# Kernel tuning notes

Measured on AMD Instinct MI355X. Metric: run time of the kernel, lower is better.

Reference implementation:

```python
import jax, jax.numpy as jnp
import numpy as np

N = 64
L = 4096
STEP = 0.001


def _make_dplr_hippo(n):
    # Standard S4 DPLR HiPPO-LegS construction (numpy, done once at setup).
    q = np.arange(n, dtype=np.float64)
    col = np.sqrt(1.0 + 2.0 * q)
    A = -(np.tril(col[:, None] * col[None, :]) - np.diag(q))
    P = np.sqrt(q + 0.5)
    B = np.sqrt(2.0 * q + 1.0)
    S = A + P[:, None] * P[None, :]
    lam_re = np.mean(np.diag(S)) * np.ones(n)
    lam_im, V = np.linalg.eigh(S * -1j)
    Pc = V.conj().T @ P
    Bc = V.conj().T @ B
    return lam_re, lam_im, Pc, Bc


def setup_inputs() -> dict:
    key = jax.random.key(0)
    k1, k2 = jax.random.split(key)
    x = jax.random.normal(k1, (16, 256, L), dtype=jnp.float32)
    lam_re, lam_im, Pc, Bc = _make_dplr_hippo(N)
    Cp = np.asarray(jax.random.normal(k2, (N, 2), dtype=jnp.float32)) * 0.5 ** 0.5
    return {
        "x": x,
        "Lambda_re": jnp.asarray(lam_re, dtype=jnp.float32),
        "Lambda_im": jnp.asarray(lam_im, dtype=jnp.float32),
        "P_re": jnp.asarray(Pc.real, dtype=jnp.float32),
        "P_im": jnp.asarray(Pc.imag, dtype=jnp.float32),
        "B_re": jnp.asarray(Bc.real, dtype=jnp.float32),
        "B_im": jnp.asarray(Bc.imag, dtype=jnp.float32),
        "C_re": jnp.asarray(Cp[:, 0], dtype=jnp.float32),
        "C_im": jnp.asarray(Cp[:, 1], dtype=jnp.float32),
    }


def _fourier_kernel(Lambda, P, B, C, step, length):
    # Frequency-domain DPLR SSM kernel (Annotated-S4 kernel_DPLR, at the roots of unity).
    Omega = jnp.exp(-2j * jnp.pi * jnp.arange(length) / length).astype(jnp.complex64)  # [L]
    g = (2.0 / step) * ((1.0 - Omega) / (1.0 + Omega))  # bilinear-transform frequencies [L]
    c = 2.0 / (1.0 + Omega)
    denom = 1.0 / (g[:, None] - Lambda[None, :])  # Cauchy matrix [L, N]
    k00 = denom @ (jnp.conj(C) * B)
    k01 = denom @ (jnp.conj(C) * P)
    k10 = denom @ (jnp.conj(P) * B)  # Q = P in this module
    k11 = denom @ (jnp.conj(P) * P)
    return c * (k00 - k01 * (1.0 / (1.0 + k11)) * k10)  # [L] complex64


def reference(x, Lambda_re, Lambda_im, P_re, P_im, B_re, B_im, C_re, C_im):
    Lambda = (Lambda_re + 1j * Lambda_im).astype(jnp.complex64)
    P = (P_re + 1j * P_im).astype(jnp.complex64)
    B = (B_re + 1j * B_im).astype(jnp.complex64)
    C = (C_re + 1j * C_im).astype(jnp.complex64)
    K = _fourier_kernel(Lambda, P, B, C, STEP, L)  # [L]
    fft_u = jnp.fft.fft(x, n=L)                    # [batch, ch, L] complex64
    y = jnp.fft.ifft(K * fft_u, n=L)
    return y.real.astype(x.dtype)
```

## Files before the change

### kernel.cpp

```cpp
#include <hip/hip_runtime.h>
#include <math.h>

#define LEN 4096
#define NSTATE 64

__device__ inline float2 cmulf(float2 a, float2 b){
  return make_float2(a.x*b.x - a.y*b.y, a.x*b.y + a.y*b.x);
}

__global__ __launch_bounds__(64)
void s4_kernelA1(const float* __restrict__ Lre, const float* __restrict__ Lim,
                 const float* __restrict__ Pre, const float* __restrict__ Pim,
                 const float* __restrict__ Bre, const float* __restrict__ Bim,
                 const float* __restrict__ Cre, const float* __restrict__ Cim,
                 float2* __restrict__ Kout) {
  const int k = blockIdx.x;
  const int n = threadIdx.x;

  double ang = -2.0 * M_PI * (double)k / (double)LEN;
  double orr = cos(ang), oi = sin(ang);
  double dr = 1.0 + orr, di = oi;
  double d2 = dr*dr + di*di;
  double nr = 1.0 - orr, ni = -oi;
  double inv_d2 = 1.0 / d2;
  double gr = 2000.0 * (nr*dr + ni*di) * inv_d2;
  double gi = 2000.0 * (ni*dr - nr*di) * inv_d2;
  double cr = 2.0 * dr * inv_d2, ci = -2.0 * di * inv_d2;

  double lr = Lre[n], li = Lim[n];
  double pr = Pre[n], pi = Pim[n];
  double br = Bre[n], bi = Bim[n];
  double qr = Cre[n], qi = Cim[n];
  double er = gr - lr, ei = gi - li;
  double inv_e2 = 1.0 / (er*er + ei*ei);
  double den_r = er * inv_e2, den_i = -ei * inv_e2;
  double cbr = qr*br + qi*bi, cbi = qr*bi - qi*br;
  double cpr = qr*pr + qi*pi, cpi = qr*pi - qi*pr;
  double pbr = pr*br + pi*bi, pbi = pr*bi - pi*br;
  double ppr = pr*pr + pi*pi;

  double k00r = den_r*cbr - den_i*cbi, k00i = den_r*cbi + den_i*cbr;
  double k01r = den_r*cpr - den_i*cpi, k01i = den_r*cpi + den_i*cpr;
  double k10r = den_r*pbr - den_i*pbi, k10i = den_r*pbi + den_i*pbr;
  double k11r = den_r*ppr,             k11i = den_i*ppr;

  #pragma unroll
  for (int off = 32; off >= 1; off >>= 1) {
    k00r += __shfl_xor(k00r, off); k00i += __shfl_xor(k00i, off);
    k01r += __shfl_xor(k01r, off); k01i += __shfl_xor(k01i, off);
    k10r += __shfl_xor(k10r, off); k10i += __shfl_xor(k10i, off);
    k11r += __shfl_xor(k11r, off); k11i += __shfl_xor(k11i, off);
  }

  if (n == 0) {
    double ar = 1.0 + k11r, ai = k11i;
    double inv_a2 = 1.0 / (ar*ar + ai*ai);
    double ivr = ar*inv_a2, ivi = -ai*inv_a2;
    double mr = k01r*k10r - k01i*k10i, mi = k01r*k10i + k01i*k10r;
    double tr = mr*ivr - mi*ivi, ti = mr*ivi + mi*ivr;
    double sr = k00r - tr, si = k00i - ti;
    double Kr = cr*sr - ci*si, Ki = cr*si + ci*sr;
    Kout[k] = make_float2((float)Kr, (float)Ki);
  }
}

__global__ void s4_kernelA2(const float2* __restrict__ Kin, float2* __restrict__ keff_br) {
  int p = blockIdx.x * blockDim.x + threadIdx.x;
  if (p >= LEN) return;
  int k = 0, pp = p;
  #pragma unroll
  for (int i = 0; i < 6; ++i) { k = (k << 2) | (pp & 3); pp >>= 2; }
  int kneg = (LEN - k) & (LEN - 1);
  float2 a = Kin[k], b = Kin[kneg];
  const float s = 0.5f / (float)LEN;
  keff_br[p] = make_float2(s * (a.x + b.x), s * (a.y - b.y));
}

__launch_bounds__(256)
__global__ void s4_fftconv(const float* __restrict__ x, const float2* __restrict__ keff_br,
                           float* __restrict__ out) {
  __shared__ float2 X[LEN];
  const int t = threadIdx.x;
  const size_t base = (size_t)blockIdx.x * 2 * LEN;
  const float* x1 = x + base;
  const float* x2 = x1 + LEN;

  #pragma unroll
  for (int i = 0; i < 16; ++i) {
    int idx = t + 256*i;
    X[idx] = make_float2(x1[idx], x2[idx]);
  }
  __syncthreads();

  for (int n = LEN; n >= 4; n >>= 2) {
    const int q = n >> 2;
    const float fac = -6.28318530717958647692f / (float)n;
    #pragma unroll
    for (int it = 0; it < 4; ++it) {
      int m = t + 256*it;
      int j = m & (q - 1);
      int i0 = 4*m - 3*j;
      float2 a0 = X[i0], a1 = X[i0+q], a2 = X[i0+2*q], a3 = X[i0+3*q];
      float2 t0 = make_float2(a0.x+a2.x, a0.y+a2.y);
      float2 t1 = make_float2(a0.x-a2.x, a0.y-a2.y);
      float2 t2 = make_float2(a1.x+a3.x, a1.y+a3.y);
      float2 t3 = make_float2(a1.x-a3.x, a1.y-a3.y);
      float2 y0 = make_float2(t0.x+t2.x, t0.y+t2.y);
      float2 y1 = make_float2(t1.x+t3.y, t1.y-t3.x);
      float2 y2 = make_float2(t0.x-t2.x, t0.y-t2.y);
      float2 y3 = make_float2(t1.x-t3.y, t1.y+t3.x);
      float ang = fac * (float)j;
      float s1, c1;
      __sincosf(ang, &s1, &c1);
      float2 w1 = make_float2(c1, s1);
      float2 w2 = cmulf(w1, w1);
      float2 w3 = cmulf(w2, w1);
      X[i0]     = y0;
      X[i0+q]   = cmulf(y1, w1);
      X[i0+2*q] = cmulf(y2, w2);
      X[i0+3*q] = cmulf(y3, w3);
    }
    __syncthreads();
  }

  #pragma unroll
  for (int it = 0; it < 4; ++it) {
    int m = t + 256*it;
    int i0 = 4*m;
    float2 u0 = cmulf(X[i0],   keff_br[i0]);
    float2 u1 = cmulf(X[i0+1], keff_br[i0+1]);
    float2 u2 = cmulf(X[i0+2], keff_br[i0+2]);
    float2 u3 = cmulf(X[i0+3], keff_br[i0+3]);
    float2 t0 = make_float2(u0.x+u2.x, u0.y+u2.y);
    float2 t1 = make_float2(u0.x-u2.x, u0.y-u2.y);
    float2 t2 = make_float2(u1.x+u3.x, u1.y+u3.y);
    float2 t3 = make_float2(u1.x-u3.x, u1.y-u3.y);
    X[i0]   = make_float2(t0.x+t2.x, t0.y+t2.y);
    X[i0+1] = make_float2(t1.x-t3.y, t1.y+t3.x);
    X[i0+2] = make_float2(t0.x-t2.x, t0.y-t2.y);
    X[i0+3] = make_float2(t1.x+t3.y, t1.y-t3.x);
  }
  __syncthreads();

  for (int n = 16; n <= LEN; n <<= 2) {
    const int q = n >> 2;
    const float fac = 6.28318530717958647692f / (float)n;
    #pragma unroll
    for (int it = 0; it < 4; ++it) {
      int m = t + 256*it;
      int j = m & (q - 1);
      int i0 = 4*m - 3*j;
      float ang = fac * (float)j;
      float s1, c1;
      __sincosf(ang, &s1, &c1);
      float2 w1 = make_float2(c1, s1);
      float2 w2 = cmulf(w1, w1);
      float2 w3 = cmulf(w2, w1);
      float2 u0 = X[i0];
      float2 u1 = cmulf(X[i0+q],   w1);
      float2 u2 = cmulf(X[i0+2*q], w2);
      float2 u3 = cmulf(X[i0+3*q], w3);
      float2 t0 = make_float2(u0.x+u2.x, u0.y+u2.y);
      float2 t1 = make_float2(u0.x-u2.x, u0.y-u2.y);
      float2 t2 = make_float2(u1.x+u3.x, u1.y+u3.y);
      float2 t3 = make_float2(u1.x-u3.x, u1.y-u3.y);
      X[i0]     = make_float2(t0.x+t2.x, t0.y+t2.y);
      X[i0+q]   = make_float2(t1.x-t3.y, t1.y+t3.x);
      X[i0+2*q] = make_float2(t0.x-t2.x, t0.y-t2.y);
      X[i0+3*q] = make_float2(t1.x+t3.y, t1.y-t3.x);
    }
    __syncthreads();
  }

  float* o1 = out + base;
  float* o2 = o1 + LEN;
  #pragma unroll
  for (int i = 0; i < 16; ++i) {
    int idx = t + 256*i;
    float2 v = X[idx];
    o1[idx] = v.x;
    o2[idx] = v.y;
  }
}

extern "C" void kernel_launch(void* const* d_in, const int* in_sizes, int n_in,
                              void* d_out, int out_size, void* d_ws, size_t ws_size,
                              hipStream_t stream) {
  const float* x   = (const float*)d_in[0];
  const float* Lre = (const float*)d_in[1];
  const float* Lim = (const float*)d_in[2];
  const float* Pre = (const float*)d_in[3];
  const float* Pim = (const float*)d_in[4];
  const float* Bre = (const float*)d_in[5];
  const float* Bim = (const float*)d_in[6];
  const float* Cre = (const float*)d_in[7];
  const float* Cim = (const float*)d_in[8];
  float* out = (float*)d_out;

  float2* Kws     = (float2*)d_ws;
  float2* keff_br = Kws + LEN;

  s4_kernelA1<<<LEN, 64, 0, stream>>>(Lre, Lim, Pre, Pim, Bre, Bim, Cre, Cim, Kws);
  s4_kernelA2<<<LEN/256, 256, 0, stream>>>(Kws, keff_br);

  const int rows = out_size / LEN;
  s4_fftconv<<<rows/2, 256, 0, stream>>>(x, keff_br, out);
}
```

Measured before the change: 160.6 us.

## Restructure FFT convolution as register-resident radix-16 passes with padded shared memory

Replaces the six radix-4 shared-memory stages per direction with three radix-16 passes done in registers. The first forward pass reads straight from global memory and the last inverse pass writes straight to global memory. The kernel multiply is fused between the third forward and first inverse DFT16. Shared memory is padded by one slot per 16 elements to avoid bank conflicts, and the keff permutation is changed to the matching digit-reversed order. This cuts barriers and shared-memory round trips, at the cost of higher register pressure from 16-element complex arrays and twiddle chains.

```diff
diff --git a/kernel.cpp b/kernel.cpp
--- a/kernel.cpp
+++ b/kernel.cpp
@@ -6,6 +6,64 @@
 
 __device__ inline float2 cmulf(float2 a, float2 b){
   return make_float2(a.x*b.x - a.y*b.y, a.x*b.y + a.y*b.x);
+}
+__device__ inline float2 cadd(float2 a, float2 b){ return make_float2(a.x+b.x, a.y+b.y); }
+__device__ inline float2 csub(float2 a, float2 b){ return make_float2(a.x-b.x, a.y-b.y); }
+
+template<bool INV>
+__device__ inline void dft16(float2 v[16]) {
+  const float C1 = 0.923879532511286756f;
+  const float S1 = 0.382683432365089772f;
+  const float R  = 0.707106781186547524f;
+  const float sg = INV ? 1.0f : -1.0f;
+  const float2 W1 = make_float2( C1,  sg*S1);
+  const float2 W2 = make_float2( R,   sg*R );
+  const float2 W3 = make_float2( S1,  sg*C1);
+  const float2 W6 = make_float2(-R,   sg*R );
+  const float2 W9 = make_float2(-C1, -sg*S1);
+
+#define BFLY4(a0,a1,a2,a3, o0,o1,o2,o3) { \
+    float2 t0 = cadd(a0,a2), t1 = csub(a0,a2); \
+    float2 t2 = cadd(a1,a3), t3 = csub(a1,a3); \
+    o0 = cadd(t0,t2); o2 = csub(t0,t2); \
+    if (!INV) { o1 = make_float2(t1.x + t3.y, t1.y - t3.x); \
+                o3 = make_float2(t1.x - t3.y, t1.y + t3.x); } \
+    else      { o1 = make_float2(t1.x - t3.y, t1.y + t3.x); \
+                o3 = make_float2(t1.x + t3.y, t1.y - t3.x); } }
+
+  float2 z[16];
+  BFLY4(v[0], v[4], v[8],  v[12], z[0], z[4], z[8],  z[12]);
+  { float2 y0,y1,y2,y3; BFLY4(v[1], v[5], v[9],  v[13], y0,y1,y2,y3);
+    z[1]=y0; z[5]=cmulf(y1,W1); z[9] =cmulf(y2,W2); z[13]=cmulf(y3,W3); }
+  { float2 y0,y1,y2,y3; BFLY4(v[2], v[6], v[10], v[14], y0,y1,y2,y3);
+    z[2]=y0; z[6]=cmulf(y1,W2);
+    z[10]= INV ? make_float2(-y2.y, y2.x) : make_float2(y2.y, -y2.x);
+    z[14]=cmulf(y3,W6); }
+  { float2 y0,y1,y2,y3; BFLY4(v[3], v[7], v[11], v[15], y0,y1,y2,y3);
+    z[3]=y0; z[7]=cmulf(y1,W3); z[11]=cmulf(y2,W6); z[15]=cmulf(y3,W9); }
+  float2 u[16];
+  BFLY4(z[0], z[1], z[2], z[3],  u[0], u[1], u[2], u[3]);
+  BFLY4(z[4], z[5], z[6], z[7],  u[4], u[5], u[6], u[7]);
+  BFLY4(z[8], z[9], z[10],z[11], u[8], u[9], u[10],u[11]);
+  BFLY4(z[12],z[13],z[14],z[15], u[12],u[13],u[14],u[15]);
+  #pragma unroll
+  for (int f = 0; f < 16; ++f) v[f] = u[((f & 3) << 2) | (f >> 2)];
+#undef BFLY4
+}
+
+__device__ inline void apply_tw(float2 v[16], float2 w1) {
+  float2 w2  = cmulf(w1,w1);
+  float2 w3  = cmulf(w2,w1);
+  float2 w4  = cmulf(w2,w2);
+  float2 w5  = cmulf(w4,w1), w6 = cmulf(w4,w2), w7 = cmulf(w4,w3);
+  float2 w8  = cmulf(w4,w4);
+  float2 w9  = cmulf(w8,w1), w10 = cmulf(w8,w2), w11 = cmulf(w8,w3);
+  float2 w12 = cmulf(w8,w4), w13 = cmulf(w8,w5), w14 = cmulf(w8,w6), w15 = cmulf(w8,w7);
+  v[1]=cmulf(v[1],w1);   v[2]=cmulf(v[2],w2);   v[3]=cmulf(v[3],w3);
+  v[4]=cmulf(v[4],w4);   v[5]=cmulf(v[5],w5);   v[6]=cmulf(v[6],w6);
+  v[7]=cmulf(v[7],w7);   v[8]=cmulf(v[8],w8);   v[9]=cmulf(v[9],w9);
+  v[10]=cmulf(v[10],w10);v[11]=cmulf(v[11],w11);v[12]=cmulf(v[12],w12);
+  v[13]=cmulf(v[13],w13);v[14]=cmulf(v[14],w14);v[15]=cmulf(v[15],w15);
 }
 
 __global__ __launch_bounds__(64)
@@ -67,119 +125,80 @@
 __global__ void s4_kernelA2(const float2* __restrict__ Kin, float2* __restrict__ keff_br) {
   int p = blockIdx.x * blockDim.x + threadIdx.x;
   if (p >= LEN) return;
-  int k = 0, pp = p;
-  #pragma unroll
-  for (int i = 0; i < 6; ++i) { k = (k << 2) | (pp & 3); pp >>= 2; }
+  int k = ((p & 15) << 8) | (p & 240) | (p >> 8);
   int kneg = (LEN - k) & (LEN - 1);
   float2 a = Kin[k], b = Kin[kneg];
   const float s = 0.5f / (float)LEN;
   keff_br[p] = make_float2(s * (a.x + b.x), s * (a.y - b.y));
 }
 
+#define PHYS(i) ((i) + ((i) >> 4))
+
 __launch_bounds__(256)
 __global__ void s4_fftconv(const float* __restrict__ x, const float2* __restrict__ keff_br,
                            float* __restrict__ out) {
-  __shared__ float2 X[LEN];
+  __shared__ float2 X[LEN + LEN/16];
   const int t = threadIdx.x;
   const size_t base = (size_t)blockIdx.x * 2 * LEN;
   const float* x1 = x + base;
   const float* x2 = x1 + LEN;
 
-  #pragma unroll
-  for (int i = 0; i < 16; ++i) {
-    int idx = t + 256*i;
-    X[idx] = make_float2(x1[idx], x2[idx]);
-  }
-  __syncthreads();
-
-  for (int n = LEN; n >= 4; n >>= 2) {
-    const int q = n >> 2;
-    const float fac = -6.28318530717958647692f / (float)n;
-    #pragma unroll
-    for (int it = 0; it < 4; ++it) {
-      int m = t + 256*it;
-      int j = m & (q - 1);
-      int i0 = 4*m - 3*j;
-      float2 a0 = X[i0], a1 = X[i0+q], a2 = X[i0+2*q], a3 = X[i0+3*q];
-      float2 t0 = make_float2(a0.x+a2.x, a0.y+a2.y);
-      float2 t1 = make_float2(a0.x-a2.x, a0.y-a2.y);
-      float2 t2 = make_float2(a1.x+a3.x, a1.y+a3.y);
-      float2 t3 = make_float2(a1.x-a3.x, a1.y-a3.y);
-      float2 y0 = make_float2(t0.x+t2.x, t0.y+t2.y);
-      float2 y1 = make_float2(t1.x+t3.y, t1.y-t3.x);
-      float2 y2 = make_float2(t0.x-t2.x, t0.y-t2.y);
-      float2 y3 = make_float2(t1.x-t3.y, t1.y+t3.x);
-      float ang = fac * (float)j;
-      float s1, c1;
-      __sincosf(ang, &s1, &c1);
-      float2 w1 = make_float2(c1, s1);
-      float2 w2 = cmulf(w1, w1);
-      float2 w3 = cmulf(w2, w1);
-      X[i0]     = y0;
-      X[i0+q]   = cmulf(y1, w1);
-      X[i0+2*q] = cmulf(y2, w2);
-      X[i0+3*q] = cmulf(y3, w3);
-    }
-    __syncthreads();
-  }
-
-  #pragma unroll
-  for (int it = 0; it < 4; ++it) {
-    int m = t + 256*it;
-    int i0 = 4*m;
-    float2 u0 = cmulf(X[i0],   keff_br[i0]);
-    float2 u1 = cmulf(X[i0+1], keff_br[i0+1]);
-    float2 u2 = cmulf(X[i0+2], keff_br[i0+2]);
-    float2 u3 = cmulf(X[i0+3], keff_br[i0+3]);
-    float2 t0 = make_float2(u0.x+u2.x, u0.y+u2.y);
-    float2 t1 = make_float2(u0.x-u2.x, u0.y-u2.y);
-    float2 t2 = make_float2(u1.x+u3.x, u1.y+u3.y);
-    float2 t3 = make_float2(u1.x-u3.x, u1.y-u3.y);
-    X[i0]   = make_float2(t0.x+t2.x, t0.y+t2.y);
-    X[i0+1] = make_float2(t1.x-t3.y, t1.y+t3.x);
-    X[i0+2] = make_float2(t0.x-t2.x, t0.y-t2.y);
-    X[i0+3] = make_float2(t1.x+t3.y, t1.y-t3.x);
-  }
-  __syncthreads();
-
-  for (int n = 16; n <= LEN; n <<= 2) {
-    const int q = n >> 2;
-    const float fac = 6.28318530717958647692f / (float)n;
-    #pragma unroll
-    for (int it = 0; it < 4; ++it) {
-      int m = t + 256*it;
-      int j = m & (q - 1);
-      int i0 = 4*m - 3*j;
-      float ang = fac * (float)j;
-      float s1, c1;
-      __sincosf(ang, &s1, &c1);
-      float2 w1 = make_float2(c1, s1);
-      float2 w2 = cmulf(w1, w1);
-      float2 w3 = cmulf(w2, w1);
-      float2 u0 = X[i0];
-      float2 u1 = cmulf(X[i0+q],   w1);
-      float2 u2 = cmulf(X[i0+2*q], w2);
-      float2 u3 = cmulf(X[i0+3*q], w3);
-      float2 t0 = make_float2(u0.x+u2.x, u0.y+u2.y);
-      float2 t1 = make_float2(u0.x-u2.x, u0.y-u2.y);
-      float2 t2 = make_float2(u1.x+u3.x, u1.y+u3.y);
-      float2 t3 = make_float2(u1.x-u3.x, u1.y-u3.y);
-      X[i0]     = make_float2(t0.x+t2.x, t0.y+t2.y);
-      X[i0+q]   = make_float2(t1.x-t3.y, t1.y+t3.x);
-      X[i0+2*q] = make_float2(t0.x-t2.x, t0.y-t2.y);
-      X[i0+3*q] = make_float2(t1.x+t3.y, t1.y-t3.x);
-    }
-    __syncthreads();
-  }
-
+  float2 v[16];
+
+  #pragma unroll
+  for (int k = 0; k < 16; ++k)
+    v[k] = make_float2(x1[t + 256*k], x2[t + 256*k]);
+  dft16<false>(v);
+  { float s_, c_;
+    __sincosf(-1.5339807878856412e-3f * (float)t, &s_, &c_);
+    apply_tw(v, make_float2(c_, s_)); }
+  #pragma unroll
+  for (int k = 0; k < 16; ++k) { int i = t + 256*k; X[PHYS(i)] = v[k]; }
+  __syncthreads();
+
+  const int i0 = ((t >> 4) << 8) + (t & 15);
+  #pragma unroll
+  for (int k = 0; k < 16; ++k) { int i = i0 + 16*k; v[k] = X[PHYS(i)]; }
+  dft16<false>(v);
+  { float s_, c_;
+    __sincosf(-2.4543692606170259e-2f * (float)(t & 15), &s_, &c_);
+    apply_tw(v, make_float2(c_, s_)); }
+  #pragma unroll
+  for (int k = 0; k < 16; ++k) { int i = i0 + 16*k; X[PHYS(i)] = v[k]; }
+  __syncthreads();
+
+  #pragma unroll
+  for (int k = 0; k < 16; ++k) v[k] = X[PHYS(16*t + k)];
+  dft16<false>(v);
+  #pragma unroll
+  for (int f = 0; f < 16; ++f) v[f] = cmulf(v[f], keff_br[16*t + f]);
+  dft16<true>(v);
+  #pragma unroll
+  for (int l = 0; l < 16; ++l) { int i = 16*t + l; X[PHYS(i)] = v[l]; }
+  __syncthreads();
+
+  #pragma unroll
+  for (int k = 0; k < 16; ++k) { int i = i0 + 16*k; v[k] = X[PHYS(i)]; }
+  { float s_, c_;
+    __sincosf(2.4543692606170259e-2f * (float)(t & 15), &s_, &c_);
+    apply_tw(v, make_float2(c_, s_)); }
+  dft16<true>(v);
+  #pragma unroll
+  for (int k = 0; k < 16; ++k) { int i = i0 + 16*k; X[PHYS(i)] = v[k]; }
+  __syncthreads();
+
+  #pragma unroll
+  for (int k = 0; k < 16; ++k) v[k] = X[PHYS(t + 256*k)];
+  { float s_, c_;
+    __sincosf(1.5339807878856412e-3f * (float)t, &s_, &c_);
+    apply_tw(v, make_float2(c_, s_)); }
+  dft16<true>(v);
   float* o1 = out + base;
   float* o2 = o1 + LEN;
   #pragma unroll
-  for (int i = 0; i < 16; ++i) {
-    int idx = t + 256*i;
-    float2 v = X[idx];
-    o1[idx] = v.x;
-    o2[idx] = v.y;
+  for (int l = 0; l < 16; ++l) {
+    o1[t + 256*l] = v[l].x;
+    o2[t + 256*l] = v[l].y;
   }
 }
 
```

After: 149.6 us. -6.8%, faster.
